# Performance work log

Measured on AMD Instinct MI355X. Metric: run time of the kernel, lower is better.

Reference implementation:

```python
import jax, jax.numpy as jnp
import numpy as np

N_NODES = 100000
N_EDGES = 1600000
N_LABEL = 100000
IN_C, H1, H2, OUT_C = 128, 128, 64, 64
MLP_H = 64


def _glorot(key, shape):
    fan_in, fan_out = shape[0], shape[1]
    s = jnp.sqrt(6.0 / (fan_in + fan_out))
    return jax.random.uniform(key, shape, jnp.float32, -s, s)


def setup_inputs() -> dict:
    key = jax.random.key(0)
    ks = jax.random.split(key, 12)
    x = jax.random.normal(ks[0], (N_NODES, IN_C), jnp.float32)
    edge_index = jax.random.randint(ks[1], (2, N_EDGES), 0, N_NODES, jnp.int64)
    edge_label_index = jax.random.randint(ks[2], (2, N_LABEL), 0, N_NODES, jnp.int64)
    return {
        "x": x,
        "edge_index": edge_index,
        "edge_label_index": edge_label_index,
        "W1": _glorot(ks[3], (IN_C, H1)), "b1": jnp.zeros((H1,), jnp.float32),
        "W2": _glorot(ks[4], (H1, H2)), "b2": jnp.zeros((H2,), jnp.float32),
        "W3": _glorot(ks[5], (H2, OUT_C)), "b3": jnp.zeros((OUT_C,), jnp.float32),
        "Wl1": _glorot(ks[6], (2 * OUT_C, MLP_H)), "bl1": jnp.zeros((MLP_H,), jnp.float32),
        "Wl2": _glorot(ks[7], (MLP_H, 1)), "bl2": jnp.zeros((1,), jnp.float32),
    }


def reference(x, edge_index, edge_label_index, W1, b1, W2, b2, W3, b3, Wl1, bl1, Wl2, bl2):
    n = x.shape[0]
    # GCNConv: add self-loops once; symmetric deg^{-1/2} normalization.
    loops = jnp.arange(n, dtype=edge_index.dtype)
    src = jnp.concatenate([edge_index[0], loops])  # [E+N]
    dst = jnp.concatenate([edge_index[1], loops])
    deg = jax.ops.segment_sum(jnp.ones_like(dst, dtype=x.dtype), dst, num_segments=n)
    deg_isqrt = jnp.where(deg > 0, jax.lax.rsqrt(jnp.maximum(deg, 1e-12)), 0.0)
    norm = deg_isqrt[src] * deg_isqrt[dst]  # [E+N]

    def conv(h, W, b):
        m = (h @ W)[src] * norm[:, None]          # gather + scale per edge
        return jax.ops.segment_sum(m, dst, num_segments=n) + b  # scatter-add

    z = jax.nn.relu(conv(x, W1, b1))   # dropout is identity at eval
    z = jax.nn.relu(conv(z, W2, b2))
    z = conv(z, W3, b3)                # [N, OUT_C]

    s, d = edge_label_index[0], edge_label_index[1]
    pairs = jnp.concatenate([z[s], z[d]], axis=1)  # [E_label, 2*OUT_C]
    h = jax.nn.relu(pairs @ Wl1 + bl1)
    logits = (h @ Wl2 + bl2)[:, 0]
    return logits
```

## Files before the change

kernel.cpp:

```cpp
#include <hip/hip_runtime.h>


typedef _Float16 half8 __attribute__((ext_vector_type(8)));
typedef float floatx4 __attribute__((ext_vector_type(4)));

#define EPB 8
#define CHUNK (256 * EPB)


__global__ __launch_bounds__(256) void k_hist_wsplit(
    const int* __restrict__ ei, int E, int n, int* __restrict__ cnt,
    const float* __restrict__ W1, _Float16* __restrict__ Wf1,
    const float* __restrict__ W2, _Float16* __restrict__ Wf2,
    const float* __restrict__ W3, _Float16* __restrict__ Wf3, int HB) {
  int b = blockIdx.x;
  if (b < HB) {
    int role = b & 7, chunk = b >> 3;
    int ns = (n + 7) / 8;
    int lo = role * ns, hi = min(n, lo + ns);
    int e0 = chunk * CHUNK + threadIdx.x;
#pragma unroll
    for (int q = 0; q < EPB; ++q) {
      int e = e0 + q * 256;
      if (e < E) {
        int d = __builtin_nontemporal_load(ei + E + e);
        if (d >= lo && d < hi) atomicAdd(&cnt[d], 1);
      }
    }
    return;
  }
  b -= HB;
  const float* W;
  _Float16* Wf;
  int KC, lc;
  if (b < 64)      { W = W1; Wf = Wf1; KC = 16384; lc = 7; }
  else if (b < 96) { b -= 64; W = W2; Wf = Wf2; KC = 8192; lc = 6; }
  else             { b -= 96; W = W3; Wf = Wf3; KC = 4096; lc = 6; }
  int t = b * 256 + threadIdx.x;
  if (t >= KC) return;
  int C = 1 << lc;
  int c = t & (C - 1), k = t >> lc;
  float a = W[t];
  _Float16 h = (_Float16)a;
  _Float16 l = (_Float16)(a - (float)h);
  int ks = k >> 5, ct = c >> 4;
  int lane = ((k & 31) >> 3) * 16 + (c & 15);
  int j = k & 7;
  int base = ((ks * (C >> 4) + ct) * 2) * 512 + lane * 8 + j;
  Wf[base] = h;
  Wf[base + 512] = l;
}


__global__ void k_scan1(const int* __restrict__ cnt, int* __restrict__ bsum, int n) {
  __shared__ int s[256];
  int i = blockIdx.x * 256 + threadIdx.x;
  int t = threadIdx.x;
  s[t] = (i < n) ? cnt[i] : 0;
  __syncthreads();
  for (int d = 128; d > 0; d >>= 1) {
    if (t < d) s[t] += s[t + d];
    __syncthreads();
  }
  if (t == 0) bsum[blockIdx.x] = s[0];
}

__global__ void k_scan2(int* __restrict__ bsum, int m, int* __restrict__ rs, int n) {
  __shared__ int s[512];
  int t = threadIdx.x;
  s[t] = (t < m) ? bsum[t] : 0;
  __syncthreads();
  for (int d = 1; d < 512; d <<= 1) {
    int v = (t >= d) ? s[t - d] : 0;
    __syncthreads();
    s[t] += v;
    __syncthreads();
  }
  if (t < m) bsum[t] = t ? s[t - 1] : 0;
  if (t == m - 1) rs[n] = s[t];
}

__global__ void k_scan3(const int* __restrict__ cnt, const int* __restrict__ bsum,
                        int* __restrict__ rs, int* __restrict__ cur,
                        float* __restrict__ isq, int n) {
  __shared__ int s[256];
  int i = blockIdx.x * 256 + threadIdx.x;
  int t = threadIdx.x;
  int v = (i < n) ? cnt[i] : 0;
  s[t] = v;
  __syncthreads();
  for (int d = 1; d < 256; d <<= 1) {
    int u = (t >= d) ? s[t - d] : 0;
    __syncthreads();
    s[t] += u;
    __syncthreads();
  }
  if (i < n) {
    int excl = bsum[blockIdx.x] + s[t] - v;
    rs[i] = excl;
    cur[i] = excl;
    isq[i] = rsqrtf((float)(v + 1));
  }
}


__global__ __launch_bounds__(256) void k_fill(const int* __restrict__ ei, int E,
                                              int n, int* __restrict__ cur,
                                              int* __restrict__ csr) {
  int role = blockIdx.x & 7, chunk = blockIdx.x >> 3;
  int ns = (n + 7) / 8;
  int lo = role * ns, hi = min(n, lo + ns);
  int e0 = chunk * CHUNK + threadIdx.x;
#pragma unroll
  for (int q = 0; q < EPB; ++q) {
    int e = e0 + q * 256;
    if (e < E) {
      int s = __builtin_nontemporal_load(ei + e);
      int d = __builtin_nontemporal_load(ei + E + e);
      if (d >= lo && d < hi) {
        int pos = atomicAdd(&cur[d], 1);
        csr[pos] = s;
      }
    }
  }
}


template <int K, int C>
__global__ __launch_bounds__(256) void k_gemm_mfma(const float* __restrict__ A,
                                                   const _Float16* __restrict__ Wf,
                                                   const float* __restrict__ isq,
                                                   _Float16* __restrict__ out, int n) {
  constexpr int NK = K / 32, NCT = C / 16;
  constexpr int WH = NK * NCT * 2 * 512;
  __shared__ __align__(16) _Float16 Wl[WH];
  int t = threadIdx.x;
  for (int i = t; i < WH / 8; i += 256)
    ((uint4*)Wl)[i] = ((const uint4*)Wf)[i];
  __syncthreads();

  int lane = t & 63, w = t >> 6;
  int rowbase = blockIdx.x * 128 + w * 32;
  int ar0 = rowbase + (lane & 15);
  int kg = (lane >> 4) * 8;

  floatx4 acc[2][NCT];
#pragma unroll
  for (int g = 0; g < 2; ++g)
#pragma unroll
    for (int ct = 0; ct < NCT; ++ct) acc[g][ct] = (floatx4){0.f, 0.f, 0.f, 0.f};

  for (int ks = 0; ks < NK; ++ks) {
    half8 ah[2], al[2];
#pragma unroll
    for (int g = 0; g < 2; ++g) {
      int row = ar0 + g * 16;
      if (row > n - 1) row = n - 1;
      const float* ap = A + (size_t)row * K + ks * 32 + kg;
      float4 u0 = ((const float4*)ap)[0];
      float4 u1 = ((const float4*)ap)[1];
      float av[8] = {u0.x, u0.y, u0.z, u0.w, u1.x, u1.y, u1.z, u1.w};
#pragma unroll
      for (int q = 0; q < 8; ++q) {
        _Float16 h = (_Float16)av[q];
        ah[g][q] = h;
        al[g][q] = (_Float16)(av[q] - (float)h);
      }
    }
#pragma unroll
    for (int ct = 0; ct < NCT; ++ct) {
      const _Float16* bp = &Wl[((ks * NCT + ct) * 2) * 512 + lane * 8];
      half8 bh = *(const half8*)bp;
      half8 bl = *(const half8*)(bp + 512);
#pragma unroll
      for (int g = 0; g < 2; ++g) {
        acc[g][ct] = __builtin_amdgcn_mfma_f32_16x16x32_f16(ah[g], bh, acc[g][ct], 0, 0, 0);
        acc[g][ct] = __builtin_amdgcn_mfma_f32_16x16x32_f16(ah[g], bl, acc[g][ct], 0, 0, 0);
        acc[g][ct] = __builtin_amdgcn_mfma_f32_16x16x32_f16(al[g], bh, acc[g][ct], 0, 0, 0);
      }
    }
  }
  int drbase = rowbase + (lane >> 4) * 4;
  int col = lane & 15;
#pragma unroll
  for (int g = 0; g < 2; ++g)
#pragma unroll
    for (int r = 0; r < 4; ++r) {
      int row = drbase + g * 16 + r;
      if (row < n) {
        float s = isq[row];
#pragma unroll
        for (int ct = 0; ct < NCT; ++ct)
          out[(size_t)row * C + ct * 16 + col] = (_Float16)(acc[g][ct][r] * s);
      }
    }
}


template <bool RELU>
__global__ __launch_bounds__(256) void k_agg128(const _Float16* __restrict__ xs,
                                                const int* __restrict__ rs,
                                                const int* __restrict__ csr,
                                                const float* __restrict__ isq,
                                                const float* __restrict__ bias,
                                                float* __restrict__ out, int n) {
  int gw = (int)((blockIdx.x * blockDim.x + threadIdx.x) >> 6);
  int lane = threadIdx.x & 63;
  if (gw >= n) return;
  int e0 = rs[gw], e1 = rs[gw + 1];
  int qtr = lane >> 4, sub = lane & 15;
  float acc[8] = {};
  int e = e0 + qtr;
  for (; e + 12 < e1; e += 16) {
    int a = __builtin_nontemporal_load(csr + e);
    int b = __builtin_nontemporal_load(csr + e + 4);
    int c = __builtin_nontemporal_load(csr + e + 8);
    int d = __builtin_nontemporal_load(csr + e + 12);
    half8 va = *(const half8*)&xs[(size_t)a * 128 + 8 * sub];
    half8 vb = *(const half8*)&xs[(size_t)b * 128 + 8 * sub];
    half8 vc = *(const half8*)&xs[(size_t)c * 128 + 8 * sub];
    half8 vd = *(const half8*)&xs[(size_t)d * 128 + 8 * sub];
#pragma unroll
    for (int j = 0; j < 8; ++j)
      acc[j] += (float)va[j] + (float)vb[j] + (float)vc[j] + (float)vd[j];
  }
  for (; e < e1; e += 4) {
    int a = __builtin_nontemporal_load(csr + e);
    half8 va = *(const half8*)&xs[(size_t)a * 128 + 8 * sub];
#pragma unroll
    for (int j = 0; j < 8; ++j) acc[j] += (float)va[j];
  }
#pragma unroll
  for (int j = 0; j < 8; ++j) {
    acc[j] += __shfl_xor(acc[j], 32, 64);
    acc[j] += __shfl_xor(acc[j], 16, 64);
  }
  if (qtr == 0) {
    float qi = isq[gw];
    half8 self = *(const half8*)&xs[(size_t)gw * 128 + 8 * sub];
#pragma unroll
    for (int j = 0; j < 8; ++j) {
      float r = qi * (acc[j] + (float)self[j]) + bias[8 * sub + j];
      if (RELU) r = fmaxf(r, 0.f);
      out[(size_t)gw * 128 + 8 * sub + j] = r;
    }
  }
}


template <bool RELU>
__global__ __launch_bounds__(256) void k_agg64(const _Float16* __restrict__ xs,
                                               const int* __restrict__ rs,
                                               const int* __restrict__ csr,
                                               const float* __restrict__ isq,
                                               const float* __restrict__ bias,
                                               float* __restrict__ out, int n) {
  int gw = (int)((blockIdx.x * blockDim.x + threadIdx.x) >> 6);
  int lane = threadIdx.x & 63;
  if (gw >= n) return;
  int e0 = rs[gw], e1 = rs[gw + 1];
  int oct = lane >> 3, sub = lane & 7;
  float acc[8] = {};
  int e = e0 + oct;
  for (; e + 8 < e1; e += 16) {
    int a = __builtin_nontemporal_load(csr + e);
    int b = __builtin_nontemporal_load(csr + e + 8);
    half8 va = *(const half8*)&xs[(size_t)a * 64 + 8 * sub];
    half8 vb = *(const half8*)&xs[(size_t)b * 64 + 8 * sub];
#pragma unroll
    for (int j = 0; j < 8; ++j) acc[j] += (float)va[j] + (float)vb[j];
  }
  for (; e < e1; e += 8) {
    int a = __builtin_nontemporal_load(csr + e);
    half8 va = *(const half8*)&xs[(size_t)a * 64 + 8 * sub];
#pragma unroll
    for (int j = 0; j < 8; ++j) acc[j] += (float)va[j];
  }
#pragma unroll
  for (int j = 0; j < 8; ++j) {
    acc[j] += __shfl_xor(acc[j], 32, 64);
    acc[j] += __shfl_xor(acc[j], 16, 64);
    acc[j] += __shfl_xor(acc[j], 8, 64);
  }
  if (oct == 0) {
    float qi = isq[gw];
    half8 self = *(const half8*)&xs[(size_t)gw * 64 + 8 * sub];
#pragma unroll
    for (int j = 0; j < 8; ++j) {
      float r = qi * (acc[j] + (float)self[j]) + bias[8 * sub + j];
      if (RELU) r = fmaxf(r, 0.f);
      out[(size_t)gw * 64 + 8 * sub + j] = r;
    }
  }
}


__global__ __launch_bounds__(256) void k_mlp(const float* __restrict__ z,
                                             const int* __restrict__ eli, int nlab,
                                             const float* __restrict__ Wl1,
                                             const float* __restrict__ bl1,
                                             const float* __restrict__ Wl2,
                                             const float* __restrict__ bl2,
                                             float* __restrict__ out) {
  constexpr int K = 128, TM = 4, LDA = K + 4;
  __shared__ float Wl[K * 64];
  __shared__ float Al[64 * LDA];
  int t = threadIdx.x;
  for (int i = t; i < K * 64 / 4; i += 256)
    ((float4*)Wl)[i] = ((const float4*)Wl1)[i];
  int rowbase = blockIdx.x * 64;
  {
    int r = t >> 2, p = t & 3;
    int row = rowbase + r;
    int idx = 0;
    if (row < nlab) idx = (p < 2) ? eli[row] : eli[nlab + row];
    const float4* src = (const float4*)(z + (size_t)idx * 64);
    int srcq = (p & 1) * 8;
    int dst = r * LDA + (p >= 2 ? 64 : 0) + (p & 1) * 32;
#pragma unroll
    for (int q = 0; q < 8; ++q)
      *(float4*)&Al[dst + 4 * q] = src[srcq + q];
  }
  __syncthreads();
  int tx = t & 15, ty = t >> 4;
  float acc[TM][4] = {};
  for (int k = 0; k < K; ++k) {
    float a[TM];
#pragma unroll
    for (int i = 0; i < TM; ++i) a[i] = Al[(ty * TM + i) * LDA + k];
    float4 w = *(const float4*)&Wl[k * 64 + tx * 4];
#pragma unroll
    for (int i = 0; i < TM; ++i) {
      acc[i][0] += a[i] * w.x;
      acc[i][1] += a[i] * w.y;
      acc[i][2] += a[i] * w.z;
      acc[i][3] += a[i] * w.w;
    }
  }
  float4 b1v = *(const float4*)&bl1[tx * 4];
  float4 w2v = *(const float4*)&Wl2[tx * 4];
  float bias2 = bl2[0];
  float part[TM];
#pragma unroll
  for (int i = 0; i < TM; ++i) {
    float h0 = fmaxf(acc[i][0] + b1v.x, 0.f);
    float h1 = fmaxf(acc[i][1] + b1v.y, 0.f);
    float h2 = fmaxf(acc[i][2] + b1v.z, 0.f);
    float h3 = fmaxf(acc[i][3] + b1v.w, 0.f);
    part[i] = h0 * w2v.x + h1 * w2v.y + h2 * w2v.z + h3 * w2v.w;
  }
#pragma unroll
  for (int i = 0; i < TM; ++i) {
#pragma unroll
    for (int m = 1; m < 16; m <<= 1)
      part[i] += __shfl_xor(part[i], m, 64);
  }
  if (tx == 0) {
#pragma unroll
    for (int i = 0; i < TM; ++i) {
      int row = rowbase + ty * TM + i;
      if (row < nlab) out[row] = part[i] + bias2;
    }
  }
}


extern "C" void kernel_launch(void* const* d_in, const int* in_sizes, int n_in,
                              void* d_out, int out_size, void* d_ws, size_t ws_size,
                              hipStream_t stream) {
  const float* x   = (const float*)d_in[0];
  const int*   ei  = (const int*)d_in[1];
  const int*   eli = (const int*)d_in[2];
  const float* W1  = (const float*)d_in[3];
  const float* b1  = (const float*)d_in[4];
  const float* W2  = (const float*)d_in[5];
  const float* b2  = (const float*)d_in[6];
  const float* W3  = (const float*)d_in[7];
  const float* b3  = (const float*)d_in[8];
  const float* Wl1 = (const float*)d_in[9];
  const float* bl1 = (const float*)d_in[10];
  const float* Wl2 = (const float*)d_in[11];
  const float* bl2 = (const float*)d_in[12];
  float* out = (float*)d_out;
  const int n    = in_sizes[0] / 128;
  const int E    = in_sizes[1] / 2;
  const int nlab = in_sizes[2] / 2;
  (void)n_in; (void)out_size; (void)ws_size;

  char* ws = (char*)d_ws;
  size_t off = 0;
  auto alloc = [&](size_t bytes) -> void* {
    void* p = ws + off;
    off = (off + bytes + 255) & ~(size_t)255;
    return p;
  };
  float*     bufZ1 = (float*)alloc((size_t)n * 128 * 4);
  float*     bufZ2 = (float*)alloc((size_t)n * 64 * 4);
  _Float16*  bufXS = (_Float16*)alloc((size_t)n * 128 * 2);
  int*       csr   = (int*)alloc((size_t)E * 4);
  int*       cnt   = (int*)alloc((size_t)n * 4);
  float*     isq   = (float*)alloc((size_t)n * 4);
  int*       rs    = (int*)alloc((size_t)(n + 1) * 4);
  int*       cur   = (int*)alloc((size_t)n * 4);
  const int  nb    = (n + 255) / 256;
  int*       bsum  = (int*)alloc((size_t)nb * 4);
  _Float16*  Wf1   = (_Float16*)alloc(128 * 128 * 2 * 2);
  _Float16*  Wf2   = (_Float16*)alloc(128 * 64 * 2 * 2);
  _Float16*  Wf3   = (_Float16*)alloc(64 * 64 * 2 * 2);
  float*     z3    = bufZ1;

  const int CH  = (E + CHUNK - 1) / CHUNK;
  const int HB  = 8 * CH;
  const int GT  = (n + 127) / 128;
  const int aggb = (n + 3) / 4;

  hipMemsetAsync(cnt, 0, (size_t)n * 4, stream);
  k_hist_wsplit<<<HB + 112, 256, 0, stream>>>(ei, E, n, cnt, W1, Wf1, W2, Wf2, W3, Wf3, HB);
  k_scan1<<<nb, 256, 0, stream>>>(cnt, bsum, n);
  k_scan2<<<1, 512, 0, stream>>>(bsum, nb, rs, n);
  k_scan3<<<nb, 256, 0, stream>>>(cnt, bsum, rs, cur, isq, n);
  k_fill<<<HB, 256, 0, stream>>>(ei, E, n, cur, csr);

  k_gemm_mfma<128, 128><<<GT, 256, 0, stream>>>(x, Wf1, isq, bufXS, n);
  k_agg128<true><<<aggb, 256, 0, stream>>>(bufXS, rs, csr, isq, b1, bufZ1, n);
  k_gemm_mfma<128, 64><<<GT, 256, 0, stream>>>(bufZ1, Wf2, isq, bufXS, n);
  k_agg64<true><<<aggb, 256, 0, stream>>>(bufXS, rs, csr, isq, b2, bufZ2, n);
  k_gemm_mfma<64, 64><<<GT, 256, 0, stream>>>(bufZ2, Wf3, isq, bufXS, n);
  k_agg64<false><<<aggb, 256, 0, stream>>>(bufXS, rs, csr, isq, b3, z3, n);
  k_mlp<<<(nlab + 63) / 64, 256, 0, stream>>>(z3, eli, nlab, Wl1, bl1, Wl2, bl2, out);
}
```

Before: 417.8 us.

## Record per-edge rank in histogram pass and fuse scan stages

```diff
diff --git a/kernel.cpp b/kernel.cpp
--- a/kernel.cpp
+++ b/kernel.cpp
@@ -10,6 +10,7 @@
 
 __global__ __launch_bounds__(256) void k_hist_wsplit(
     const int* __restrict__ ei, int E, int n, int* __restrict__ cnt,
+    unsigned short* __restrict__ rank,
     const float* __restrict__ W1, _Float16* __restrict__ Wf1,
     const float* __restrict__ W2, _Float16* __restrict__ Wf2,
     const float* __restrict__ W3, _Float16* __restrict__ Wf3, int HB) {
@@ -24,7 +25,10 @@
       int e = e0 + q * 256;
       if (e < E) {
         int d = __builtin_nontemporal_load(ei + E + e);
-        if (d >= lo && d < hi) atomicAdd(&cnt[d], 1);
+        if (d >= lo && d < hi) {
+          int r = atomicAdd(&cnt[d], 1);
+          rank[e] = (unsigned short)r;
+        }
       }
     }
     return;
@@ -65,27 +69,26 @@
   if (t == 0) bsum[blockIdx.x] = s[0];
 }
 
-__global__ void k_scan2(int* __restrict__ bsum, int m, int* __restrict__ rs, int n) {
-  __shared__ int s[512];
+__global__ void k_scan23(const int* __restrict__ cnt, const int* __restrict__ bsum,
+                         int nb, int* __restrict__ rs, float* __restrict__ isq,
+                         int n) {
+  __shared__ int s[256];
+  __shared__ int off;
   int t = threadIdx.x;
-  s[t] = (t < m) ? bsum[t] : 0;
-  __syncthreads();
-  for (int d = 1; d < 512; d <<= 1) {
-    int v = (t >= d) ? s[t - d] : 0;
+  int b = blockIdx.x;
+  int acc = 0;
+  for (int j = t; j < b; j += 256) acc += bsum[j];
+  s[t] = acc;
+  __syncthreads();
+  for (int d = 128; d > 0; d >>= 1) {
+    if (t < d) s[t] += s[t + d];
     __syncthreads();
-    s[t] += v;
-    __syncthreads();
-  }
-  if (t < m) bsum[t] = t ? s[t - 1] : 0;
-  if (t == m - 1) rs[n] = s[t];
-}
-
-__global__ void k_scan3(const int* __restrict__ cnt, const int* __restrict__ bsum,
-                        int* __restrict__ rs, int* __restrict__ cur,
-                        float* __restrict__ isq, int n) {
-  __shared__ int s[256];
-  int i = blockIdx.x * 256 + threadIdx.x;
-  int t = threadIdx.x;
+  }
+  if (t == 0) off = s[0];
+  __syncthreads();
+  int blockoff = off;
+  __syncthreads();
+  int i = b * 256 + t;
   int v = (i < n) ? cnt[i] : 0;
   s[t] = v;
   __syncthreads();
@@ -96,16 +99,17 @@
     __syncthreads();
   }
   if (i < n) {
-    int excl = bsum[blockIdx.x] + s[t] - v;
+    int excl = blockoff + s[t] - v;
     rs[i] = excl;
-    cur[i] = excl;
     isq[i] = rsqrtf((float)(v + 1));
+    if (i == n - 1) rs[n] = excl + v;
   }
 }
 
 
 __global__ __launch_bounds__(256) void k_fill(const int* __restrict__ ei, int E,
-                                              int n, int* __restrict__ cur,
+                                              int n, const int* __restrict__ rs,
+                                              const unsigned short* __restrict__ rank,
                                               int* __restrict__ csr) {
   int role = blockIdx.x & 7, chunk = blockIdx.x >> 3;
   int ns = (n + 7) / 8;
@@ -115,11 +119,11 @@
   for (int q = 0; q < EPB; ++q) {
     int e = e0 + q * 256;
     if (e < E) {
-      int s = __builtin_nontemporal_load(ei + e);
       int d = __builtin_nontemporal_load(ei + E + e);
       if (d >= lo && d < hi) {
-        int pos = atomicAdd(&cur[d], 1);
-        csr[pos] = s;
+        int s = __builtin_nontemporal_load(ei + e);
+        int r = __builtin_nontemporal_load(rank + e);
+        csr[rs[d] + r] = s;
       }
     }
   }
@@ -398,10 +402,10 @@
   float*     bufZ2 = (float*)alloc((size_t)n * 64 * 4);
   _Float16*  bufXS = (_Float16*)alloc((size_t)n * 128 * 2);
   int*       csr   = (int*)alloc((size_t)E * 4);
+  unsigned short* rank = (unsigned short*)alloc((size_t)E * 2);
   int*       cnt   = (int*)alloc((size_t)n * 4);
   float*     isq   = (float*)alloc((size_t)n * 4);
   int*       rs    = (int*)alloc((size_t)(n + 1) * 4);
-  int*       cur   = (int*)alloc((size_t)n * 4);
   const int  nb    = (n + 255) / 256;
   int*       bsum  = (int*)alloc((size_t)nb * 4);
   _Float16*  Wf1   = (_Float16*)alloc(128 * 128 * 2 * 2);
@@ -415,11 +419,11 @@
   const int aggb = (n + 3) / 4;
 
   hipMemsetAsync(cnt, 0, (size_t)n * 4, stream);
-  k_hist_wsplit<<<HB + 112, 256, 0, stream>>>(ei, E, n, cnt, W1, Wf1, W2, Wf2, W3, Wf3, HB);
+  k_hist_wsplit<<<HB + 112, 256, 0, stream>>>(ei, E, n, cnt, rank,
+                                              W1, Wf1, W2, Wf2, W3, Wf3, HB);
   k_scan1<<<nb, 256, 0, stream>>>(cnt, bsum, n);
-  k_scan2<<<1, 512, 0, stream>>>(bsum, nb, rs, n);
-  k_scan3<<<nb, 256, 0, stream>>>(cnt, bsum, rs, cur, isq, n);
-  k_fill<<<HB, 256, 0, stream>>>(ei, E, n, cur, csr);
+  k_scan23<<<nb, 256, 0, stream>>>(cnt, bsum, nb, rs, isq, n);
+  k_fill<<<HB, 256, 0, stream>>>(ei, E, n, rs, rank, csr);
 
   k_gemm_mfma<128, 128><<<GT, 256, 0, stream>>>(x, Wf1, isq, bufXS, n);
   k_agg128<true><<<aggb, 256, 0, stream>>>(bufXS, rs, csr, isq, b1, bufZ1, n);
```

After: 395.2 us. -5.4%, faster.
